# Performance work log

Measured on AMD Instinct MI355X. Metric: run time of the kernel, lower is better.

Reference implementation:

```python
import jax, jax.numpy as jnp
import numpy as np

# Dimensions
B, LQ, HQ, HKV, D = 4, 512, 16, 8, 128          # seqs, q tokens/seq, q heads, kv heads, head dim
BLOCK_SIZE, BLOCKS_PER_SEQ, NUM_BLOCKS = 256, 8, 64  # paged KV-cache geometry
CTX = BLOCK_SIZE * BLOCKS_PER_SEQ                # cached tokens per seq (full blocks, rem=0)
LK = CTX + LQ                                    # keys per seq = cache + current step
DIFF_BLOCK = 128                                 # diffusion block: bidirectional inside, causal across
SCALE = 1.0 / float(np.sqrt(D))


def _make_allow_mask():
    # True = allowed to attend. All cached tokens visible; within the current
    # step, query attends up to the end of its own diffusion block (block-causal,
    # intra-block bidirectional) -- the semantics described in the module docstring.
    qi = jnp.arange(LQ)
    kj = jnp.arange(LK)
    limit = CTX + ((qi // DIFF_BLOCK) + 1) * DIFF_BLOCK   # [LQ]
    m = kj[None, :] < limit[:, None]                      # [LQ, LK]
    return jnp.broadcast_to(m[None], (B, LQ, LK))


def setup_inputs() -> dict:
    key = jax.random.key(0)
    ks = jax.random.split(key, 6)
    q = jax.random.normal(ks[0], (B, LQ, HQ, D), jnp.float32)
    k = jax.random.normal(ks[1], (B, LQ, HKV, D), jnp.float32)
    v = jax.random.normal(ks[2], (B, LQ, HKV, D), jnp.float32)
    k_cache = jax.random.normal(ks[3], (NUM_BLOCKS, BLOCK_SIZE, HKV, D), jnp.float32)
    v_cache = jax.random.normal(ks[4], (NUM_BLOCKS, BLOCK_SIZE, HKV, D), jnp.float32)
    # distinct physical block slots per sequence (as a paged allocator would give)
    block_tables = jax.random.permutation(ks[5], NUM_BLOCKS)[: B * BLOCKS_PER_SEQ]
    block_tables = block_tables.reshape(B, BLOCKS_PER_SEQ).astype(jnp.int32)
    allow_mask = _make_allow_mask()
    return dict(q=q, k=k, v=v, k_cache=k_cache, v_cache=v_cache,
                block_tables=block_tables, allow_mask=allow_mask)


def reference(q, k, v, k_cache, v_cache, block_tables, allow_mask):
    rep = HQ // HKV
    # paged gather: [B, nblk, blk, Hkv, D] -> [B, CTX, Hkv, D]
    K_ctx = k_cache[block_tables].reshape(B, CTX, HKV, D)
    V_ctx = v_cache[block_tables].reshape(B, CTX, HKV, D)
    K_all = jnp.concatenate([K_ctx, k], axis=1)   # [B, LK, Hkv, D]
    V_all = jnp.concatenate([V_ctx, v], axis=1)
    # GQA: repeat_interleave kv heads to q heads
    K_all = jnp.repeat(K_all, rep, axis=2)        # [B, LK, Hq, D]
    V_all = jnp.repeat(V_all, rep, axis=2)
    scores = jnp.einsum('bqhd,bkhd->bhqk', q * SCALE, K_all)  # [B, Hq, LQ, LK]
    neg = jnp.finfo(scores.dtype).min
    scores = jnp.where(allow_mask[:, None, :, :], scores, neg)
    attn = jax.nn.softmax(scores, axis=-1)
    return jnp.einsum('bhqk,bkhd->bqhd', attn, V_all)         # [B, LQ, Hq, D]
```

## Files before the change

### kernel.cpp

```cpp
#include <hip/hip_runtime.h>
#include <hip/hip_bf16.h>


#define B_    4
#define LQ_   512
#define HQ_   16
#define HKV_  8
#define D_    128
#define BLKSZ_ 256
#define BPS_  8
#define CTX_  2048
#define DIFFB_ 128
#define KT_   64
#define SCALE_ 0.08838834764831845f

typedef __attribute__((ext_vector_type(4))) float f32x4;
typedef __attribute__((ext_vector_type(8))) short bf16x8;
typedef __attribute__((ext_vector_type(2))) unsigned u32x2;

__device__ __forceinline__ unsigned cvt_pk2(float a, float b) {
  union { __hip_bfloat162 h; unsigned u; } x;
  x.h = __float22bfloat162_rn(float2{a, b});
  return x.u;
}
union bf8u { bf16x8 v; unsigned u[4]; };

__device__ __forceinline__ int kidx(int kv, int d) {
  return kv * 128 + ((((d >> 3) ^ kv) & 15) << 3) + (d & 7);
}
__device__ __forceinline__ int vidx(int d, int p) {
  return d * 64 + ((((p >> 3) ^ d ^ (d >> 3)) & 7) << 3) + (p & 7);
}
__device__ __forceinline__ int pkmap(int kv) {
  return ((kv & 12) << 2) | ((kv & 48) >> 2) | (kv & 3);
}

__global__ __launch_bounds__(512, 2)
void block_attn_kernel(const float* __restrict__ qg,
                       const float* __restrict__ kcur,
                       const float* __restrict__ vcur,
                       const float* __restrict__ kcache,
                       const float* __restrict__ vcache,
                       const int*   __restrict__ btab,
                       float*       __restrict__ out) {
  const int blk  = blockIdx.x;
  const int hkv  = blk & 7;
  const int b    = (blk >> 3) & 3;
  const int qb   = blk >> 5;
  const int tid  = threadIdx.x;
  const int lane = tid & 63;
  const int wave = tid >> 6;
  const int lo   = lane & 15;
  const int hi   = lane >> 4;
  const int nt   = (CTX_ + (qb / 2 + 1) * DIFFB_) / KT_;

  __shared__ __align__(16) short Kl[2][KT_ * D_];
  __shared__ __align__(16) short Vl[2][D_ * KT_];

  if (wave < 4) {
    const int hq    = hkv * 2 + (wave >> 1);
    const int qrow0 = qb * 64 + (wave & 1) * 32;

    bf16x8 qf[2][4];
#pragma unroll
    for (int sub = 0; sub < 2; ++sub) {
      const float* qr = qg + ((size_t)((b * LQ_ + qrow0 + sub * 16 + lo)) * HQ_ + hq) * D_;
#pragma unroll
      for (int db = 0; db < 4; ++db) {
        const int d0 = db * 32 + hi * 8;
        f32x4 a  = *(const f32x4*)(qr + d0);
        f32x4 c4 = *(const f32x4*)(qr + d0 + 4);
        bf8u f;
        f.u[0] = cvt_pk2(a[0] * SCALE_, a[1] * SCALE_);
        f.u[1] = cvt_pk2(a[2] * SCALE_, a[3] * SCALE_);
        f.u[2] = cvt_pk2(c4[0] * SCALE_, c4[1] * SCALE_);
        f.u[3] = cvt_pk2(c4[2] * SCALE_, c4[3] * SCALE_);
        qf[sub][db] = f.v;
      }
    }

    f32x4 oacc[2][8];
#pragma unroll
    for (int s = 0; s < 2; ++s)
#pragma unroll
      for (int i = 0; i < 8; ++i) oacc[s][i] = (f32x4){0.f, 0.f, 0.f, 0.f};
    float mrow[2] = {-1e30f, -1e30f}, lrow[2] = {0.f, 0.f};

    __syncthreads();

    for (int t = 0; t < nt; ++t) {
      const short* Kb = Kl[t & 1];
      const short* Vb = Vl[t & 1];

      f32x4 sacc[2][4];
#pragma unroll
      for (int s = 0; s < 2; ++s)
#pragma unroll
        for (int cs = 0; cs < 4; ++cs) sacc[s][cs] = (f32x4){0.f, 0.f, 0.f, 0.f};
#pragma unroll
      for (int cs = 0; cs < 4; ++cs) {
#pragma unroll
        for (int db = 0; db < 4; ++db) {
          bf16x8 kf = *(const bf16x8*)&Kb[kidx(cs * 16 + lo, db * 32 + hi * 8)];
          sacc[0][cs] = __builtin_amdgcn_mfma_f32_16x16x32_bf16(kf, qf[0][db], sacc[0][cs], 0, 0, 0);
          sacc[1][cs] = __builtin_amdgcn_mfma_f32_16x16x32_bf16(kf, qf[1][db], sacc[1][cs], 0, 0, 0);
        }
      }

      bf16x8 pa[2][2];
#pragma unroll
      for (int sub = 0; sub < 2; ++sub) {
        float m0 = fmaxf(fmaxf(sacc[sub][0][0], sacc[sub][0][1]),
                         fmaxf(sacc[sub][0][2], sacc[sub][0][3]));
        float m1 = fmaxf(fmaxf(sacc[sub][1][0], sacc[sub][1][1]),
                         fmaxf(sacc[sub][1][2], sacc[sub][1][3]));
        float m2 = fmaxf(fmaxf(sacc[sub][2][0], sacc[sub][2][1]),
                         fmaxf(sacc[sub][2][2], sacc[sub][2][3]));
        float m3 = fmaxf(fmaxf(sacc[sub][3][0], sacc[sub][3][1]),
                         fmaxf(sacc[sub][3][2], sacc[sub][3][3]));
        float mx = fmaxf(fmaxf(m0, m1), fmaxf(m2, m3));
        mx = fmaxf(mx, __shfl_xor(mx, 16));
        mx = fmaxf(mx, __shfl_xor(mx, 32));
        const bool keep = __all(mx - mrow[sub] <= 8.0f);
        const float mnew = keep ? mrow[sub] : fmaxf(mrow[sub], mx);
        float rs = 0.f;
#pragma unroll
        for (int cs = 0; cs < 4; ++cs)
#pragma unroll
          for (int i = 0; i < 4; ++i) {
            const float p = __expf(sacc[sub][cs][i] - mnew);
            sacc[sub][cs][i] = p;
            rs += p;
          }
        rs += __shfl_xor(rs, 16);
        rs += __shfl_xor(rs, 32);
        if (keep) {
          lrow[sub] += rs;
        } else {
          const float sc = __expf(mrow[sub] - mnew);
          lrow[sub] = lrow[sub] * sc + rs;
          mrow[sub] = mnew;
#pragma unroll
          for (int dt = 0; dt < 8; ++dt) oacc[sub][dt] *= sc;
        }
#pragma unroll
        for (int ch = 0; ch < 2; ++ch) {
          bf8u p;
          p.u[0] = cvt_pk2(sacc[sub][2 * ch][0],     sacc[sub][2 * ch][1]);
          p.u[1] = cvt_pk2(sacc[sub][2 * ch][2],     sacc[sub][2 * ch][3]);
          p.u[2] = cvt_pk2(sacc[sub][2 * ch + 1][0], sacc[sub][2 * ch + 1][1]);
          p.u[3] = cvt_pk2(sacc[sub][2 * ch + 1][2], sacc[sub][2 * ch + 1][3]);
          pa[sub][ch] = p.v;
        }
      }

#pragma unroll
      for (int ch = 0; ch < 2; ++ch) {
#pragma unroll
        for (int dt = 0; dt < 8; ++dt) {
          bf16x8 vf = *(const bf16x8*)&Vb[vidx(dt * 16 + lo, hi * 16 + ch * 8)];
          oacc[0][dt] = __builtin_amdgcn_mfma_f32_16x16x32_bf16(vf, pa[0][ch], oacc[0][dt], 0, 0, 0);
          oacc[1][dt] = __builtin_amdgcn_mfma_f32_16x16x32_bf16(vf, pa[1][ch], oacc[1][dt], 0, 0, 0);
        }
      }

      __syncthreads();
    }

#pragma unroll
    for (int sub = 0; sub < 2; ++sub) {
      const float inv = 1.f / lrow[sub];
      float* orow = out + ((size_t)(b * LQ_ + qrow0 + sub * 16 + lo) * HQ_ + hq) * D_;
#pragma unroll
      for (int dt = 0; dt < 8; ++dt) {
        f32x4 o4 = oacc[sub][dt] * inv;
        *(f32x4*)(orow + dt * 16 + hi * 4) = o4;
      }
    }
  } else {
    const int pid = tid & 255;
    const int cK  = pid >> 4;
    const int e   = pid & 15;
    const int qd  = pid >> 4;
    const int dc  = pid & 15;
    const int r0v = qd * 4;
    const int d0v = dc * 8;
    const int P0v = pkmap(r0v);
    f32x4 kreg[4][2], vreg[4][2];

    auto issue_loads = [&](int t) {
      const int kbase = t * KT_;
      const float *kb_, *vb_;
      if (kbase < CTX_) {
        const int pb = btab[b * BPS_ + (kbase >> 8)];
        const size_t base = ((size_t)(pb * BLKSZ_ + (kbase & 255)) * HKV_ + hkv) * D_;
        kb_ = kcache + base; vb_ = vcache + base;
      } else {
        const size_t base = ((size_t)(b * LQ_ + (kbase - CTX_)) * HKV_ + hkv) * D_;
        kb_ = kcur + base;  vb_ = vcur + base;
      }
      const size_t rs = (size_t)HKV_ * D_;
#pragma unroll
      for (int i = 0; i < 4; ++i) {
        const float* kr = kb_ + (size_t)(cK + 16 * i) * rs + e * 8;
        kreg[i][0] = *(const f32x4*)(kr);
        kreg[i][1] = *(const f32x4*)(kr + 4);
      }
#pragma unroll
      for (int m = 0; m < 4; ++m) {
        const float* vr = vb_ + (size_t)(r0v + m) * rs + d0v;
        vreg[m][0] = *(const f32x4*)(vr);
        vreg[m][1] = *(const f32x4*)(vr + 4);
      }
    };

    auto write_lds = [&](int bsel) {
      short* Kb = Kl[bsel];
      short* Vb = Vl[bsel];
#pragma unroll
      for (int i = 0; i < 4; ++i) {
        bf8u f;
        f.u[0] = cvt_pk2(kreg[i][0][0], kreg[i][0][1]);
        f.u[1] = cvt_pk2(kreg[i][0][2], kreg[i][0][3]);
        f.u[2] = cvt_pk2(kreg[i][1][0], kreg[i][1][1]);
        f.u[3] = cvt_pk2(kreg[i][1][2], kreg[i][1][3]);
        *(bf16x8*)&Kb[kidx(cK + 16 * i, e * 8)] = f.v;
      }
#pragma unroll
      for (int j = 0; j < 8; ++j) {
        u32x2 w;
        w[0] = cvt_pk2(vreg[0][j >> 2][j & 3], vreg[1][j >> 2][j & 3]);
        w[1] = cvt_pk2(vreg[2][j >> 2][j & 3], vreg[3][j >> 2][j & 3]);
        *(u32x2*)&Vb[vidx(d0v + j, P0v)] = w;
      }
    };

    issue_loads(0);
    write_lds(0);
    if (nt > 1) issue_loads(1);
    asm volatile("s_waitcnt lgkmcnt(0)" ::: "memory");
    __builtin_amdgcn_s_barrier();

    for (int t = 0; t < nt; ++t) {
      if (t + 1 < nt) write_lds((t + 1) & 1);
      if (t + 2 < nt) issue_loads(t + 2);
      asm volatile("s_waitcnt lgkmcnt(0)" ::: "memory");
      __builtin_amdgcn_s_barrier();
    }
  }
}

extern "C" void kernel_launch(void* const* d_in, const int* in_sizes, int n_in,
                              void* d_out, int out_size, void* d_ws, size_t ws_size,
                              hipStream_t stream) {
  (void)in_sizes; (void)n_in; (void)out_size; (void)d_ws; (void)ws_size;
  const float* q      = (const float*)d_in[0];
  const float* k      = (const float*)d_in[1];
  const float* v      = (const float*)d_in[2];
  const float* kcache = (const float*)d_in[3];
  const float* vcache = (const float*)d_in[4];
  const int*   btab   = (const int*)d_in[5];
  float* out = (float*)d_out;

  block_attn_kernel<<<dim3(B_ * HKV_ * (LQ_ / 64)), dim3(512), 0, stream>>>(
      q, k, v, kcache, vcache, btab, out);
}
```

Baseline: 73.86 us.

## Software-pipeline QK and PV across tiles with triple-buffered V and exp2 softmax

Restructures the consumer loop so the PV product of tile t-1 is issued together with the QK product of tile t. The softmax of tile t then runs after both, which lets MFMA work overlap the exp and reduction work. To make this safe, V is triple-buffered in LDS. The log2(e) factor is folded into the Q scale so exp2f can be used. The row sum is now accumulated by an extra MFMA against a ones vector instead of shuffle reductions, and s_setprio raises wave priority around the MFMA phases. The costs are more LDS, which may limit occupancy, and two extra MFMAs per tile.

```diff
diff --git a/kernel.cpp b/kernel.cpp
--- a/kernel.cpp
+++ b/kernel.cpp
@@ -12,7 +12,8 @@
 #define CTX_  2048
 #define DIFFB_ 128
 #define KT_   64
-#define SCALE_ 0.08838834764831845f
+#define SCALE2_ 0.1275174457576656f
+#define THR2_   11.541560327111707f
 
 typedef __attribute__((ext_vector_type(4))) float f32x4;
 typedef __attribute__((ext_vector_type(8))) short bf16x8;
@@ -24,6 +25,10 @@
   return x.u;
 }
 union bf8u { bf16x8 v; unsigned u[4]; };
+
+__device__ __forceinline__ float fmax3f(float a, float b, float c) {
+  return fmaxf(fmaxf(a, b), c);
+}
 
 __device__ __forceinline__ int kidx(int kv, int d) {
   return kv * 128 + ((((d >> 3) ^ kv) & 15) << 3) + (d & 7);
@@ -55,7 +60,7 @@
   const int nt   = (CTX_ + (qb / 2 + 1) * DIFFB_) / KT_;
 
   __shared__ __align__(16) short Kl[2][KT_ * D_];
-  __shared__ __align__(16) short Vl[2][D_ * KT_];
+  __shared__ __align__(16) short Vl[3][KT_ * D_];
 
   if (wave < 4) {
     const int hq    = hkv * 2 + (wave >> 1);
@@ -71,10 +76,10 @@
         f32x4 a  = *(const f32x4*)(qr + d0);
         f32x4 c4 = *(const f32x4*)(qr + d0 + 4);
         bf8u f;
-        f.u[0] = cvt_pk2(a[0] * SCALE_, a[1] * SCALE_);
-        f.u[1] = cvt_pk2(a[2] * SCALE_, a[3] * SCALE_);
-        f.u[2] = cvt_pk2(c4[0] * SCALE_, c4[1] * SCALE_);
-        f.u[3] = cvt_pk2(c4[2] * SCALE_, c4[3] * SCALE_);
+        f.u[0] = cvt_pk2(a[0] * SCALE2_, a[1] * SCALE2_);
+        f.u[1] = cvt_pk2(a[2] * SCALE2_, a[3] * SCALE2_);
+        f.u[2] = cvt_pk2(c4[0] * SCALE2_, c4[1] * SCALE2_);
+        f.u[3] = cvt_pk2(c4[2] * SCALE2_, c4[3] * SCALE2_);
         qf[sub][db] = f.v;
       }
     }
@@ -84,76 +89,28 @@
     for (int s = 0; s < 2; ++s)
 #pragma unroll
       for (int i = 0; i < 8; ++i) oacc[s][i] = (f32x4){0.f, 0.f, 0.f, 0.f};
-    float mrow[2] = {-1e30f, -1e30f}, lrow[2] = {0.f, 0.f};
-
-    __syncthreads();
-
-    for (int t = 0; t < nt; ++t) {
-      const short* Kb = Kl[t & 1];
-      const short* Vb = Vl[t & 1];
-
-      f32x4 sacc[2][4];
-#pragma unroll
-      for (int s = 0; s < 2; ++s)
-#pragma unroll
-        for (int cs = 0; cs < 4; ++cs) sacc[s][cs] = (f32x4){0.f, 0.f, 0.f, 0.f};
-#pragma unroll
-      for (int cs = 0; cs < 4; ++cs) {
+    f32x4 oaccL[2] = {(f32x4){0.f, 0.f, 0.f, 0.f}, (f32x4){0.f, 0.f, 0.f, 0.f}};
+    float mrow[2] = {-1e30f, -1e30f};
+    bf16x8 pa[2][2];
+    bf16x8 ones;
+    {
+      bf8u o;
+      o.u[0] = o.u[1] = o.u[2] = o.u[3] = 0x3F803F80u;
+      ones = o.v;
+    }
+
+    auto QK = [&](const short* Kb, f32x4 (&sacc)[2][4]) {
+#pragma unroll
+      for (int cs = 0; cs < 4; ++cs)
 #pragma unroll
         for (int db = 0; db < 4; ++db) {
           bf16x8 kf = *(const bf16x8*)&Kb[kidx(cs * 16 + lo, db * 32 + hi * 8)];
           sacc[0][cs] = __builtin_amdgcn_mfma_f32_16x16x32_bf16(kf, qf[0][db], sacc[0][cs], 0, 0, 0);
           sacc[1][cs] = __builtin_amdgcn_mfma_f32_16x16x32_bf16(kf, qf[1][db], sacc[1][cs], 0, 0, 0);
         }
-      }
-
-      bf16x8 pa[2][2];
-#pragma unroll
-      for (int sub = 0; sub < 2; ++sub) {
-        float m0 = fmaxf(fmaxf(sacc[sub][0][0], sacc[sub][0][1]),
-                         fmaxf(sacc[sub][0][2], sacc[sub][0][3]));
-        float m1 = fmaxf(fmaxf(sacc[sub][1][0], sacc[sub][1][1]),
-                         fmaxf(sacc[sub][1][2], sacc[sub][1][3]));
-        float m2 = fmaxf(fmaxf(sacc[sub][2][0], sacc[sub][2][1]),
-                         fmaxf(sacc[sub][2][2], sacc[sub][2][3]));
-        float m3 = fmaxf(fmaxf(sacc[sub][3][0], sacc[sub][3][1]),
-                         fmaxf(sacc[sub][3][2], sacc[sub][3][3]));
-        float mx = fmaxf(fmaxf(m0, m1), fmaxf(m2, m3));
-        mx = fmaxf(mx, __shfl_xor(mx, 16));
-        mx = fmaxf(mx, __shfl_xor(mx, 32));
-        const bool keep = __all(mx - mrow[sub] <= 8.0f);
-        const float mnew = keep ? mrow[sub] : fmaxf(mrow[sub], mx);
-        float rs = 0.f;
-#pragma unroll
-        for (int cs = 0; cs < 4; ++cs)
-#pragma unroll
-          for (int i = 0; i < 4; ++i) {
-            const float p = __expf(sacc[sub][cs][i] - mnew);
-            sacc[sub][cs][i] = p;
-            rs += p;
-          }
-        rs += __shfl_xor(rs, 16);
-        rs += __shfl_xor(rs, 32);
-        if (keep) {
-          lrow[sub] += rs;
-        } else {
-          const float sc = __expf(mrow[sub] - mnew);
-          lrow[sub] = lrow[sub] * sc + rs;
-          mrow[sub] = mnew;
-#pragma unroll
-          for (int dt = 0; dt < 8; ++dt) oacc[sub][dt] *= sc;
-        }
-#pragma unroll
-        for (int ch = 0; ch < 2; ++ch) {
-          bf8u p;
-          p.u[0] = cvt_pk2(sacc[sub][2 * ch][0],     sacc[sub][2 * ch][1]);
-          p.u[1] = cvt_pk2(sacc[sub][2 * ch][2],     sacc[sub][2 * ch][3]);
-          p.u[2] = cvt_pk2(sacc[sub][2 * ch + 1][0], sacc[sub][2 * ch + 1][1]);
-          p.u[3] = cvt_pk2(sacc[sub][2 * ch + 1][2], sacc[sub][2 * ch + 1][3]);
-          pa[sub][ch] = p.v;
-        }
-      }
-
+    };
+
+    auto PV = [&](const short* Vb) {
 #pragma unroll
       for (int ch = 0; ch < 2; ++ch) {
 #pragma unroll
@@ -162,14 +119,82 @@
           oacc[0][dt] = __builtin_amdgcn_mfma_f32_16x16x32_bf16(vf, pa[0][ch], oacc[0][dt], 0, 0, 0);
           oacc[1][dt] = __builtin_amdgcn_mfma_f32_16x16x32_bf16(vf, pa[1][ch], oacc[1][dt], 0, 0, 0);
         }
-      }
-
+        oaccL[0] = __builtin_amdgcn_mfma_f32_16x16x32_bf16(ones, pa[0][ch], oaccL[0], 0, 0, 0);
+        oaccL[1] = __builtin_amdgcn_mfma_f32_16x16x32_bf16(ones, pa[1][ch], oaccL[1], 0, 0, 0);
+      }
+    };
+
+    auto SM = [&](f32x4 (&s)[2][4]) {
+#pragma unroll
+      for (int sub = 0; sub < 2; ++sub) {
+        float x0 = fmax3f(s[sub][0][0], s[sub][0][1], s[sub][0][2]);
+        float x1 = fmax3f(s[sub][0][3], s[sub][1][0], s[sub][1][1]);
+        float x2 = fmax3f(s[sub][1][2], s[sub][1][3], s[sub][2][0]);
+        float x3 = fmax3f(s[sub][2][1], s[sub][2][2], s[sub][2][3]);
+        float x4 = fmax3f(s[sub][3][0], s[sub][3][1], s[sub][3][2]);
+        float mx = fmaxf(fmax3f(x0, x1, x2), fmax3f(x3, x4, s[sub][3][3]));
+        mx = fmaxf(mx, __shfl_xor(mx, 16));
+        mx = fmaxf(mx, __shfl_xor(mx, 32));
+        const bool keep = __all(mx - mrow[sub] <= THR2_);
+        if (!keep) {
+          const float mnew = fmaxf(mrow[sub], mx);
+          const float sc = exp2f(mrow[sub] - mnew);
+          mrow[sub] = mnew;
+#pragma unroll
+          for (int dt = 0; dt < 8; ++dt) oacc[sub][dt] *= sc;
+          oaccL[sub] *= sc;
+        }
+        const float m = mrow[sub];
+#pragma unroll
+        for (int cs = 0; cs < 4; ++cs)
+#pragma unroll
+          for (int i = 0; i < 4; ++i)
+            s[sub][cs][i] = exp2f(s[sub][cs][i] - m);
+#pragma unroll
+        for (int ch = 0; ch < 2; ++ch) {
+          bf8u p;
+          p.u[0] = cvt_pk2(s[sub][2 * ch][0],     s[sub][2 * ch][1]);
+          p.u[1] = cvt_pk2(s[sub][2 * ch][2],     s[sub][2 * ch][3]);
+          p.u[2] = cvt_pk2(s[sub][2 * ch + 1][0], s[sub][2 * ch + 1][1]);
+          p.u[3] = cvt_pk2(s[sub][2 * ch + 1][2], s[sub][2 * ch + 1][3]);
+          pa[sub][ch] = p.v;
+        }
+      }
+    };
+
+    __syncthreads();
+    {
+      f32x4 sacc[2][4];
+#pragma unroll
+      for (int s2 = 0; s2 < 2; ++s2)
+#pragma unroll
+        for (int cs = 0; cs < 4; ++cs) sacc[s2][cs] = (f32x4){0.f, 0.f, 0.f, 0.f};
+      __builtin_amdgcn_s_setprio(1);
+      QK(Kl[0], sacc);
+      __builtin_amdgcn_s_setprio(0);
+      SM(sacc);
+    }
+    for (int t = 1; t < nt; ++t) {
       __syncthreads();
-    }
+      f32x4 sacc[2][4];
+#pragma unroll
+      for (int s2 = 0; s2 < 2; ++s2)
+#pragma unroll
+        for (int cs = 0; cs < 4; ++cs) sacc[s2][cs] = (f32x4){0.f, 0.f, 0.f, 0.f};
+      __builtin_amdgcn_s_setprio(1);
+      QK(Kl[t & 1], sacc);
+      PV(Vl[(t - 1) % 3]);
+      __builtin_amdgcn_s_setprio(0);
+      SM(sacc);
+    }
+    __syncthreads();
+    __builtin_amdgcn_s_setprio(1);
+    PV(Vl[(nt - 1) % 3]);
+    __builtin_amdgcn_s_setprio(0);
 
 #pragma unroll
     for (int sub = 0; sub < 2; ++sub) {
-      const float inv = 1.f / lrow[sub];
+      const float inv = 1.f / oaccL[sub][0];
       float* orow = out + ((size_t)(b * LQ_ + qrow0 + sub * 16 + lo) * HQ_ + hq) * D_;
 #pragma unroll
       for (int dt = 0; dt < 8; ++dt) {
@@ -214,9 +239,9 @@
       }
     };
 
-    auto write_lds = [&](int bsel) {
-      short* Kb = Kl[bsel];
-      short* Vb = Vl[bsel];
+    auto write_lds = [&](int t) {
+      short* Kb = Kl[t & 1];
+      short* Vb = Vl[t % 3];
 #pragma unroll
       for (int i = 0; i < 4; ++i) {
         bf8u f;
@@ -242,7 +267,7 @@
     __builtin_amdgcn_s_barrier();
 
     for (int t = 0; t < nt; ++t) {
-      if (t + 1 < nt) write_lds((t + 1) & 1);
+      if (t + 1 < nt) write_lds(t + 1);
       if (t + 2 < nt) issue_loads(t + 2);
       asm volatile("s_waitcnt lgkmcnt(0)" ::: "memory");
       __builtin_amdgcn_s_barrier();
```

New measurement: 81.63 us. +10.5%, slower.

## Fold log2e into Q scale, use exp2, compute row sums via MFMA

Applied to the files above, without the earlier changes.

The Q scale now includes log2(e), so the softmax uses exp2f directly and the rescale threshold is adjusted to match. The per-row sum of probabilities is no longer reduced with adds and cross-lane shuffles. It is accumulated by an extra MFMA against a vector of bf16 ones. The max reduction is regrouped into three-input max operations. The aim is to cut VALU and shuffle work in the softmax, at the cost of two extra MFMAs per chunk and a row sum built from bf16-rounded probabilities.

```diff
diff --git a/kernel.cpp b/kernel.cpp
--- a/kernel.cpp
+++ b/kernel.cpp
@@ -12,7 +12,8 @@
 #define CTX_  2048
 #define DIFFB_ 128
 #define KT_   64
-#define SCALE_ 0.08838834764831845f
+#define SCALE2_ 0.1275174457576656f
+#define THR2_   11.541560327111707f
 
 typedef __attribute__((ext_vector_type(4))) float f32x4;
 typedef __attribute__((ext_vector_type(8))) short bf16x8;
@@ -24,6 +25,10 @@
   return x.u;
 }
 union bf8u { bf16x8 v; unsigned u[4]; };
+
+__device__ __forceinline__ float fmax3f(float a, float b, float c) {
+  return fmaxf(fmaxf(a, b), c);
+}
 
 __device__ __forceinline__ int kidx(int kv, int d) {
   return kv * 128 + ((((d >> 3) ^ kv) & 15) << 3) + (d & 7);
@@ -71,10 +76,10 @@
         f32x4 a  = *(const f32x4*)(qr + d0);
         f32x4 c4 = *(const f32x4*)(qr + d0 + 4);
         bf8u f;
-        f.u[0] = cvt_pk2(a[0] * SCALE_, a[1] * SCALE_);
-        f.u[1] = cvt_pk2(a[2] * SCALE_, a[3] * SCALE_);
-        f.u[2] = cvt_pk2(c4[0] * SCALE_, c4[1] * SCALE_);
-        f.u[3] = cvt_pk2(c4[2] * SCALE_, c4[3] * SCALE_);
+        f.u[0] = cvt_pk2(a[0] * SCALE2_, a[1] * SCALE2_);
+        f.u[1] = cvt_pk2(a[2] * SCALE2_, a[3] * SCALE2_);
+        f.u[2] = cvt_pk2(c4[0] * SCALE2_, c4[1] * SCALE2_);
+        f.u[3] = cvt_pk2(c4[2] * SCALE2_, c4[3] * SCALE2_);
         qf[sub][db] = f.v;
       }
     }
@@ -84,7 +89,14 @@
     for (int s = 0; s < 2; ++s)
 #pragma unroll
       for (int i = 0; i < 8; ++i) oacc[s][i] = (f32x4){0.f, 0.f, 0.f, 0.f};
-    float mrow[2] = {-1e30f, -1e30f}, lrow[2] = {0.f, 0.f};
+    f32x4 oaccL[2] = {(f32x4){0.f, 0.f, 0.f, 0.f}, (f32x4){0.f, 0.f, 0.f, 0.f}};
+    float mrow[2] = {-1e30f, -1e30f};
+    bf16x8 ones;
+    {
+      bf8u o;
+      o.u[0] = o.u[1] = o.u[2] = o.u[3] = 0x3F803F80u;
+      ones = o.v;
+    }
 
     __syncthreads();
 
@@ -110,39 +122,29 @@
       bf16x8 pa[2][2];
 #pragma unroll
       for (int sub = 0; sub < 2; ++sub) {
-        float m0 = fmaxf(fmaxf(sacc[sub][0][0], sacc[sub][0][1]),
-                         fmaxf(sacc[sub][0][2], sacc[sub][0][3]));
-        float m1 = fmaxf(fmaxf(sacc[sub][1][0], sacc[sub][1][1]),
-                         fmaxf(sacc[sub][1][2], sacc[sub][1][3]));
-        float m2 = fmaxf(fmaxf(sacc[sub][2][0], sacc[sub][2][1]),
-                         fmaxf(sacc[sub][2][2], sacc[sub][2][3]));
-        float m3 = fmaxf(fmaxf(sacc[sub][3][0], sacc[sub][3][1]),
-                         fmaxf(sacc[sub][3][2], sacc[sub][3][3]));
-        float mx = fmaxf(fmaxf(m0, m1), fmaxf(m2, m3));
+        float x0 = fmax3f(sacc[sub][0][0], sacc[sub][0][1], sacc[sub][0][2]);
+        float x1 = fmax3f(sacc[sub][0][3], sacc[sub][1][0], sacc[sub][1][1]);
+        float x2 = fmax3f(sacc[sub][1][2], sacc[sub][1][3], sacc[sub][2][0]);
+        float x3 = fmax3f(sacc[sub][2][1], sacc[sub][2][2], sacc[sub][2][3]);
+        float x4 = fmax3f(sacc[sub][3][0], sacc[sub][3][1], sacc[sub][3][2]);
+        float mx = fmaxf(fmax3f(x0, x1, x2), fmax3f(x3, x4, sacc[sub][3][3]));
         mx = fmaxf(mx, __shfl_xor(mx, 16));
         mx = fmaxf(mx, __shfl_xor(mx, 32));
-        const bool keep = __all(mx - mrow[sub] <= 8.0f);
-        const float mnew = keep ? mrow[sub] : fmaxf(mrow[sub], mx);
-        float rs = 0.f;
+        const bool keep = __all(mx - mrow[sub] <= THR2_);
+        if (!keep) {
+          const float mnew = fmaxf(mrow[sub], mx);
+          const float sc = exp2f(mrow[sub] - mnew);
+          mrow[sub] = mnew;
+#pragma unroll
+          for (int dt = 0; dt < 8; ++dt) oacc[sub][dt] *= sc;
+          oaccL[sub] *= sc;
+        }
+        const float m = mrow[sub];
 #pragma unroll
         for (int cs = 0; cs < 4; ++cs)
 #pragma unroll
-          for (int i = 0; i < 4; ++i) {
-            const float p = __expf(sacc[sub][cs][i] - mnew);
-            sacc[sub][cs][i] = p;
-            rs += p;
-          }
-        rs += __shfl_xor(rs, 16);
-        rs += __shfl_xor(rs, 32);
-        if (keep) {
-          lrow[sub] += rs;
-        } else {
-          const float sc = __expf(mrow[sub] - mnew);
-          lrow[sub] = lrow[sub] * sc + rs;
-          mrow[sub] = mnew;
-#pragma unroll
-          for (int dt = 0; dt < 8; ++dt) oacc[sub][dt] *= sc;
-        }
+          for (int i = 0; i < 4; ++i)
+            sacc[sub][cs][i] = exp2f(sacc[sub][cs][i] - m);
 #pragma unroll
         for (int ch = 0; ch < 2; ++ch) {
           bf8u p;
@@ -162,6 +164,8 @@
           oacc[0][dt] = __builtin_amdgcn_mfma_f32_16x16x32_bf16(vf, pa[0][ch], oacc[0][dt], 0, 0, 0);
           oacc[1][dt] = __builtin_amdgcn_mfma_f32_16x16x32_bf16(vf, pa[1][ch], oacc[1][dt], 0, 0, 0);
         }
+        oaccL[0] = __builtin_amdgcn_mfma_f32_16x16x32_bf16(ones, pa[0][ch], oaccL[0], 0, 0, 0);
+        oaccL[1] = __builtin_amdgcn_mfma_f32_16x16x32_bf16(ones, pa[1][ch], oaccL[1], 0, 0, 0);
       }
 
       __syncthreads();
@@ -169,7 +173,7 @@
 
 #pragma unroll
     for (int sub = 0; sub < 2; ++sub) {
-      const float inv = 1.f / lrow[sub];
+      const float inv = 1.f / oaccL[sub][0];
       float* orow = out + ((size_t)(b * LQ_ + qrow0 + sub * 16 + lo) * HQ_ + hq) * D_;
 #pragma unroll
       for (int dt = 0; dt < 8; ++dt) {
```

Result: slower. 81.75 us (+10.7%).

## Split each KV tile across two consumer waves and merge partial softmax results

Applied to the files above, without the earlier changes.

Doubles the consumer waves from four to eight, with each pair splitting the 64-key tile into two 32-key halves. Each wave keeps its own running max, sum and output accumulator, and the pair merges them at the end through shared memory. The V-packing permutation changes to match the new half-tile P fragment layout. The block grows to 768 threads and the launch-bounds occupancy hint is dropped, which may cut blocks per CU. The end-of-kernel merge adds an extra barrier and shared-memory traffic.

```diff
diff --git a/kernel.cpp b/kernel.cpp
--- a/kernel.cpp
+++ b/kernel.cpp
@@ -31,11 +31,11 @@
 __device__ __forceinline__ int vidx(int d, int p) {
   return d * 64 + ((((p >> 3) ^ d ^ (d >> 3)) & 7) << 3) + (p & 7);
 }
-__device__ __forceinline__ int pkmap(int kv) {
-  return ((kv & 12) << 2) | ((kv & 48) >> 2) | (kv & 3);
-}
-
-__global__ __launch_bounds__(512, 2)
+__device__ __forceinline__ int pk32(int w) {
+  return (((w >> 2) & 3) << 3) | (((w >> 4) & 1) << 2) | (w & 3);
+}
+
+__global__ __launch_bounds__(768)
 void block_attn_kernel(const float* __restrict__ qg,
                        const float* __restrict__ kcur,
                        const float* __restrict__ vcur,
@@ -54,12 +54,15 @@
   const int hi   = lane >> 4;
   const int nt   = (CTX_ + (qb / 2 + 1) * DIFFB_) / KT_;
 
-  __shared__ __align__(16) short Kl[2][KT_ * D_];
-  __shared__ __align__(16) short Vl[2][D_ * KT_];
-
-  if (wave < 4) {
-    const int hq    = hkv * 2 + (wave >> 1);
-    const int qrow0 = qb * 64 + (wave & 1) * 32;
+  __shared__ __align__(16) char smem[65536];
+  __shared__ float ms[8][16], ls[8][16];
+  float* Os = (float*)smem;
+
+  if (wave < 8) {
+    const int kvh  = wave & 1;
+    const int g    = wave >> 1;
+    const int hq    = hkv * 2 + (g >> 1);
+    const int qrow0 = qb * 64 + (g & 1) * 32;
 
     bf16x8 qf[2][4];
 #pragma unroll
@@ -89,43 +92,40 @@
     __syncthreads();
 
     for (int t = 0; t < nt; ++t) {
-      const short* Kb = Kl[t & 1];
-      const short* Vb = Vl[t & 1];
-
-      f32x4 sacc[2][4];
+      const short* Kb = (const short*)(smem + (t & 1) * 16384);
+      const short* Vb = (const short*)(smem + 32768 + (t & 1) * 16384);
+
+      f32x4 sacc[2][2];
 #pragma unroll
       for (int s = 0; s < 2; ++s)
 #pragma unroll
-        for (int cs = 0; cs < 4; ++cs) sacc[s][cs] = (f32x4){0.f, 0.f, 0.f, 0.f};
-#pragma unroll
-      for (int cs = 0; cs < 4; ++cs) {
+        for (int cs = 0; cs < 2; ++cs) sacc[s][cs] = (f32x4){0.f, 0.f, 0.f, 0.f};
+#pragma unroll
+      for (int cs = 0; cs < 2; ++cs) {
 #pragma unroll
         for (int db = 0; db < 4; ++db) {
-          bf16x8 kf = *(const bf16x8*)&Kb[kidx(cs * 16 + lo, db * 32 + hi * 8)];
+          bf16x8 kf = *(const bf16x8*)&Kb[kidx(kvh * 32 + cs * 16 + lo,
+                                               db * 32 + hi * 8)];
           sacc[0][cs] = __builtin_amdgcn_mfma_f32_16x16x32_bf16(kf, qf[0][db], sacc[0][cs], 0, 0, 0);
           sacc[1][cs] = __builtin_amdgcn_mfma_f32_16x16x32_bf16(kf, qf[1][db], sacc[1][cs], 0, 0, 0);
         }
       }
 
-      bf16x8 pa[2][2];
+      bf16x8 pa[2];
 #pragma unroll
       for (int sub = 0; sub < 2; ++sub) {
         float m0 = fmaxf(fmaxf(sacc[sub][0][0], sacc[sub][0][1]),
                          fmaxf(sacc[sub][0][2], sacc[sub][0][3]));
         float m1 = fmaxf(fmaxf(sacc[sub][1][0], sacc[sub][1][1]),
                          fmaxf(sacc[sub][1][2], sacc[sub][1][3]));
-        float m2 = fmaxf(fmaxf(sacc[sub][2][0], sacc[sub][2][1]),
-                         fmaxf(sacc[sub][2][2], sacc[sub][2][3]));
-        float m3 = fmaxf(fmaxf(sacc[sub][3][0], sacc[sub][3][1]),
-                         fmaxf(sacc[sub][3][2], sacc[sub][3][3]));
-        float mx = fmaxf(fmaxf(m0, m1), fmaxf(m2, m3));
+        float mx = fmaxf(m0, m1);
         mx = fmaxf(mx, __shfl_xor(mx, 16));
         mx = fmaxf(mx, __shfl_xor(mx, 32));
         const bool keep = __all(mx - mrow[sub] <= 8.0f);
         const float mnew = keep ? mrow[sub] : fmaxf(mrow[sub], mx);
         float rs = 0.f;
 #pragma unroll
-        for (int cs = 0; cs < 4; ++cs)
+        for (int cs = 0; cs < 2; ++cs)
 #pragma unroll
           for (int i = 0; i < 4; ++i) {
             const float p = __expf(sacc[sub][cs][i] - mnew);
@@ -143,38 +143,50 @@
 #pragma unroll
           for (int dt = 0; dt < 8; ++dt) oacc[sub][dt] *= sc;
         }
-#pragma unroll
-        for (int ch = 0; ch < 2; ++ch) {
-          bf8u p;
-          p.u[0] = cvt_pk2(sacc[sub][2 * ch][0],     sacc[sub][2 * ch][1]);
-          p.u[1] = cvt_pk2(sacc[sub][2 * ch][2],     sacc[sub][2 * ch][3]);
-          p.u[2] = cvt_pk2(sacc[sub][2 * ch + 1][0], sacc[sub][2 * ch + 1][1]);
-          p.u[3] = cvt_pk2(sacc[sub][2 * ch + 1][2], sacc[sub][2 * ch + 1][3]);
-          pa[sub][ch] = p.v;
+        bf8u p;
+        p.u[0] = cvt_pk2(sacc[sub][0][0], sacc[sub][0][1]);
+        p.u[1] = cvt_pk2(sacc[sub][0][2], sacc[sub][0][3]);
+        p.u[2] = cvt_pk2(sacc[sub][1][0], sacc[sub][1][1]);
+        p.u[3] = cvt_pk2(sacc[sub][1][2], sacc[sub][1][3]);
+        pa[sub] = p.v;
+      }
+
+#pragma unroll
+      for (int dt = 0; dt < 8; ++dt) {
+        bf16x8 vf = *(const bf16x8*)&Vb[vidx(dt * 16 + lo, kvh * 32 + hi * 8)];
+        oacc[0][dt] = __builtin_amdgcn_mfma_f32_16x16x32_bf16(vf, pa[0], oacc[0][dt], 0, 0, 0);
+        oacc[1][dt] = __builtin_amdgcn_mfma_f32_16x16x32_bf16(vf, pa[1], oacc[1][dt], 0, 0, 0);
+      }
+
+      __syncthreads();
+    }
+
+    if (kvh == 1) {
+#pragma unroll
+      for (int sub = 0; sub < 2; ++sub) {
+#pragma unroll
+        for (int dt = 0; dt < 8; ++dt)
+          *(f32x4*)&Os[(size_t)(g * 32 + sub * 16 + lo) * 128 + dt * 16 + hi * 4] =
+              oacc[sub][dt];
+        if (hi == 0) { ms[g * 2 + sub][lo] = mrow[sub]; ls[g * 2 + sub][lo] = lrow[sub]; }
+      }
+    }
+    __syncthreads();
+    if (kvh == 0) {
+#pragma unroll
+      for (int sub = 0; sub < 2; ++sub) {
+        const float m1 = ms[g * 2 + sub][lo], l1 = ls[g * 2 + sub][lo];
+        const float mstar = fmaxf(mrow[sub], m1);
+        const float a0 = __expf(mrow[sub] - mstar);
+        const float a1 = __expf(m1 - mstar);
+        const float linv = 1.f / (lrow[sub] * a0 + l1 * a1);
+        float* orow = out + ((size_t)(b * LQ_ + qrow0 + sub * 16 + lo) * HQ_ + hq) * D_;
+#pragma unroll
+        for (int dt = 0; dt < 8; ++dt) {
+          f32x4 o1 = *(const f32x4*)&Os[(size_t)(g * 32 + sub * 16 + lo) * 128 + dt * 16 + hi * 4];
+          f32x4 o = (oacc[sub][dt] * a0 + o1 * a1) * linv;
+          *(f32x4*)(orow + dt * 16 + hi * 4) = o;
         }
-      }
-
-#pragma unroll
-      for (int ch = 0; ch < 2; ++ch) {
-#pragma unroll
-        for (int dt = 0; dt < 8; ++dt) {
-          bf16x8 vf = *(const bf16x8*)&Vb[vidx(dt * 16 + lo, hi * 16 + ch * 8)];
-          oacc[0][dt] = __builtin_amdgcn_mfma_f32_16x16x32_bf16(vf, pa[0][ch], oacc[0][dt], 0, 0, 0);
-          oacc[1][dt] = __builtin_amdgcn_mfma_f32_16x16x32_bf16(vf, pa[1][ch], oacc[1][dt], 0, 0, 0);
-        }
-      }
-
-      __syncthreads();
-    }
-
-#pragma unroll
-    for (int sub = 0; sub < 2; ++sub) {
-      const float inv = 1.f / lrow[sub];
-      float* orow = out + ((size_t)(b * LQ_ + qrow0 + sub * 16 + lo) * HQ_ + hq) * D_;
-#pragma unroll
-      for (int dt = 0; dt < 8; ++dt) {
-        f32x4 o4 = oacc[sub][dt] * inv;
-        *(f32x4*)(orow + dt * 16 + hi * 4) = o4;
       }
     }
   } else {
@@ -185,7 +197,7 @@
     const int dc  = pid & 15;
     const int r0v = qd * 4;
     const int d0v = dc * 8;
-    const int P0v = pkmap(r0v);
+    const int P0v = (r0v & 32) + pk32(r0v & 31);
     f32x4 kreg[4][2], vreg[4][2];
 
     auto issue_loads = [&](int t) {
@@ -215,8 +227,8 @@
     };
 
     auto write_lds = [&](int bsel) {
-      short* Kb = Kl[bsel];
-      short* Vb = Vl[bsel];
+      short* Kb = (short*)(smem + bsel * 16384);
+      short* Vb = (short*)(smem + 32768 + bsel * 16384);
 #pragma unroll
       for (int i = 0; i < 4; ++i) {
         bf8u f;
@@ -247,6 +259,7 @@
       asm volatile("s_waitcnt lgkmcnt(0)" ::: "memory");
       __builtin_amdgcn_s_barrier();
     }
+    __builtin_amdgcn_s_barrier();
   }
 }
 
@@ -262,6 +275,6 @@
   const int*   btab   = (const int*)d_in[5];
   float* out = (float*)d_out;
 
-  block_attn_kernel<<<dim3(B_ * HKV_ * (LQ_ / 64)), dim3(512), 0, stream>>>(
+  block_attn_kernel<<<dim3(B_ * HKV_ * (LQ_ / 64)), dim3(768), 0, stream>>>(
       q, k, v, kcache, vcache, btab, out);
 }
```

After: 81.18 us. 1.1x slower.
